# Performance work log

Measured on AMD Instinct MI355X. Metric: run time of the kernel, lower is better.

The kernel has to match this reference:

```python
import jax, jax.numpy as jnp
import numpy as np

NUM_HEADS = 8

def dwconv(x, w, b, pad):
    # depthwise conv: x [B, C, H, W], w [C, 1, k, k], groups=C
    y = jax.lax.conv_general_dilated(
        x, w, window_strides=(1, 1), padding=[(pad, pad), (pad, pad)],
        feature_group_count=x.shape[1], dimension_numbers=('NCHW', 'OIHW', 'NCHW'))
    return y + b[None, :, None, None]


def setup_inputs() -> dict:
    key = jax.random.key(0)
    ks = jax.random.split(key, 12)
    B, H, W = 32, 28, 28
    C = 512
    N = 1 + H * W
    Ch = C // NUM_HEADS  # 64
    s = lambda k, shp, fan: jax.random.normal(k, shp, jnp.float32) * (fan ** -0.5)
    return {
        'x': jax.random.normal(ks[0], (B, N, C), jnp.float32),
        'qkv_w': s(ks[1], (3 * C, C), C),
        'qkv_b': jnp.zeros((3 * C,), jnp.float32),
        'proj_w': s(ks[2], (C, C), C),
        'proj_b': jnp.zeros((C,), jnp.float32),
        'w3': s(ks[3], (2 * Ch, 1, 3, 3), 9),
        'b3': jnp.zeros((2 * Ch,), jnp.float32),
        'w5': s(ks[4], (3 * Ch, 1, 5, 5), 25),
        'b5': jnp.zeros((3 * Ch,), jnp.float32),
        'w7': s(ks[5], (3 * Ch, 1, 7, 7), 49),
        'b7': jnp.zeros((3 * Ch,), jnp.float32),
        'H': H,
        'W': W,
    }


def reference(x, qkv_w, qkv_b, proj_w, proj_b, w3, b3, w5, b5, w7, b7, H, W):
    B, N, C = x.shape
    h = NUM_HEADS
    Ch = C // h
    scale = Ch ** -0.5
    # qkv projection -> q, k, v each [B, h, N, Ch]
    qkv = (x @ qkv_w.T + qkv_b).reshape(B, N, 3, h, Ch).transpose(2, 0, 3, 1, 4)
    q, k, v = qkv[0], qkv[1], qkv[2]
    # factorized attention: softmax over tokens on k, then (k^T v) then q @ ...
    k_sm = jax.nn.softmax(k, axis=2)
    kv = jnp.einsum('bhnc,bhnd->bhcd', k_sm, v)          # [B,h,Ch,Ch]
    factor_att = jnp.einsum('bhnc,bhcd->bhnd', q, kv)    # [B,h,N,Ch]
    # conv relative position encoding (CRPE) on image tokens only
    q_img = q[:, :, 1:, :]                               # [B,h,HW,Ch]
    v_img = v[:, :, 1:, :].transpose(0, 1, 3, 2).reshape(B, h * Ch, H, W)
    splits = np.cumsum([2 * Ch, 3 * Ch, 3 * Ch])[:-1]
    v1, v2, v3 = jnp.split(v_img, splits, axis=1)
    conv_v = jnp.concatenate(
        [dwconv(v1, w3, b3, 1), dwconv(v2, w5, b5, 2), dwconv(v3, w7, b7, 3)], axis=1)
    conv_v = conv_v.reshape(B, h, Ch, H * W).transpose(0, 1, 3, 2)  # [B,h,HW,Ch]
    EV = q_img * conv_v
    crpe = jnp.pad(EV, ((0, 0), (0, 0), (1, 0), (0, 0)))  # zero row for cls token
    out = scale * factor_att + crpe
    out = out.transpose(0, 2, 1, 3).reshape(B, N, C)
    return out @ proj_w.T + proj_b
```

## Files before the change

### kernel.cpp

```cpp
#include <hip/hip_runtime.h>
#include <cstdint>
#include <cstddef>


typedef unsigned short u16;

#define HEADS 8
#define CHD   64
#define CDIM  512
#define NTOK  785
#define BATCH 32
#define MROWS (BATCH * NTOK)
#define MPAD  25344
#define QKVN  1536
#define IMGHW 784
#define KVSPLIT 7

typedef float  f32x4  __attribute__((ext_vector_type(4)));
typedef __bf16 bf16x8 __attribute__((ext_vector_type(8)));

__device__ __forceinline__ u16 f2bf(float f) {
  union { float f; uint32_t u; } x; x.f = f;
  uint32_t r = x.u + 0x7fffu + ((x.u >> 16) & 1u);
  return (u16)(r >> 16);
}
__device__ __forceinline__ float bf2f(u16 u) {
  union { uint32_t u; float f; } x; x.u = ((uint32_t)u) << 16;
  return x.f;
}
__device__ __forceinline__ float bflo(uint32_t u) { return bf2f((u16)(u & 0xffffu)); }
__device__ __forceinline__ float bfhi(uint32_t u) { return bf2f((u16)(u >> 16)); }
__device__ __forceinline__ uint32_t pk2(float a, float b) {
#if __has_builtin(__builtin_amdgcn_cvt_pk_bf16_f32)
  auto v = __builtin_amdgcn_cvt_pk_bf16_f32(a, b);
  union { decltype(v) v2; uint32_t u; } cv; cv.v2 = v; return cv.u;
#else
  return (uint32_t)f2bf(a) | ((uint32_t)f2bf(b) << 16);
#endif
}

__global__ __launch_bounds__(256)
void casts_kernel(const float* __restrict__ x, u16* __restrict__ xb,
                  const float* __restrict__ w1, u16* __restrict__ w1b,
                  const float* __restrict__ w2, u16* __restrict__ w2b) {
  const int N1 = MROWS * CDIM / 4, N2 = QKVN * CDIM / 4, N3 = CDIM * CDIM / 4;
  int i = blockIdx.x * 256 + threadIdx.x;
  const float* src; u16* dst;
  if (i < N1)           { src = x;  dst = xb;  }
  else if (i < N1 + N2) { i -= N1;  src = w1; dst = w1b; }
  else if (i < N1 + N2 + N3) { i -= N1 + N2; src = w2; dst = w2b; }
  else return;
  float4 v = reinterpret_cast<const float4*>(src)[i];
  uint2 o; o.x = pk2(v.x, v.y); o.y = pk2(v.z, v.w);
  reinterpret_cast<uint2*>(dst)[i] = o;
}

__device__ __forceinline__ void gld_lds16(const u16* g, u16* l) {
  __builtin_amdgcn_global_load_lds((__attribute__((address_space(1))) void*)g,
                                   (__attribute__((address_space(3))) void*)l,
                                   16, 0, 0);
}

template <int OUTBF16>
__global__ __launch_bounds__(512)
void gemm_bt(const u16* __restrict__ A, const u16* __restrict__ W,
             const float* __restrict__ bias, void* __restrict__ Cout,
             int Mstore, int N, int K, int nMt, int nNt) {
  __shared__ __align__(16) u16 lsA[2][256 * 32];
  __shared__ __align__(16) u16 lsB[2][128 * 32];
  const int flat = blockIdx.x;
  const int xcd = flat & 7, idx = flat >> 3;
  const int nt = idx % nNt;
  const int mt = (idx / nNt) * 8 + xcd;
  if (mt >= nMt) return;
  const int tile_m = mt * 256, tile_n = nt * 128;

  const int tid  = threadIdx.x;
  const int wave = tid >> 6, lane = tid & 63;
  const int quad = lane >> 4, l16 = lane & 15;
  const int wm = (wave & 3) * 64, wn = (wave >> 2) * 64;

  const int srow = tid >> 2;
  const int scol = ((tid & 3) ^ ((tid >> 3) & 3)) * 8;
  const int ldst = tid * 8;

  auto stage = [&](int kt, int buf) {
    const int kc = kt * 32 + scol;
#pragma unroll
    for (int s = 0; s < 2; ++s)
      gld_lds16(A + (size_t)(tile_m + s * 128 + srow) * K + kc,
                &lsA[buf][s * 4096 + ldst]);
    gld_lds16(W + (size_t)(tile_n + srow) * K + kc, &lsB[buf][ldst]);
  };

  f32x4 acc[4][4] = {};

  stage(0, 0);
  __syncthreads();

  const int KT = K >> 5;
  const int pch = (quad ^ ((l16 >> 1) & 3)) * 8;
#pragma unroll 2
  for (int t = 0; t < KT; ++t) {
    const int cur = t & 1;
    if (t + 1 < KT) stage(t + 1, cur ^ 1);
    bf16x8 af[4], bfr[4];
#pragma unroll
    for (int i = 0; i < 4; ++i) {
      af[i]  = *reinterpret_cast<const bf16x8*>(
          &lsA[cur][(wm + i * 16 + l16) * 32 + pch]);
      bfr[i] = *reinterpret_cast<const bf16x8*>(
          &lsB[cur][(wn + i * 16 + l16) * 32 + pch]);
    }
#pragma unroll
    for (int i = 0; i < 4; ++i)
#pragma unroll
      for (int j = 0; j < 4; ++j)
        acc[i][j] = __builtin_amdgcn_mfma_f32_16x16x32_bf16(
            af[i], bfr[j], acc[i][j], 0, 0, 0);
    __syncthreads();
  }

#pragma unroll
  for (int i = 0; i < 4; ++i) {
    const int mbase = tile_m + wm + i * 16 + quad * 4;
#pragma unroll
    for (int j = 0; j < 4; ++j) {
      const int n  = tile_n + wn + j * 16 + l16;
      const float bv = bias[n];
      const float v0 = acc[i][j][0] + bv, v1 = acc[i][j][1] + bv;
      const float v2 = acc[i][j][2] + bv, v3 = acc[i][j][3] + bv;
      if (OUTBF16) {
        u16* cp = reinterpret_cast<u16*>(Cout) + (size_t)mbase * N + n;
        const uint32_t p01 = pk2(v0, v1), p23 = pk2(v2, v3);
        if (mbase + 0 < Mstore) cp[0]            = (u16)p01;
        if (mbase + 1 < Mstore) cp[(size_t)N]    = (u16)(p01 >> 16);
        if (mbase + 2 < Mstore) cp[(size_t)N*2]  = (u16)p23;
        if (mbase + 3 < Mstore) cp[(size_t)N*3]  = (u16)(p23 >> 16);
      } else {
        float* cp = reinterpret_cast<float*>(Cout) + (size_t)mbase * N + n;
        if (mbase + 0 < Mstore) cp[0]           = v0;
        if (mbase + 1 < Mstore) cp[(size_t)N]   = v1;
        if (mbase + 2 < Mstore) cp[(size_t)N*2] = v2;
        if (mbase + 3 < Mstore) cp[(size_t)N*3] = v3;
      }
    }
  }
}

__device__ __forceinline__ void kv_part(
    const u16* __restrict__ qkv, float* __restrict__ kvpart,
    float* __restrict__ kvsum, int bh, int split,
    float* __restrict__ e_s, float* __restrict__ v_s) {
  const int b = bh >> 3, h = bh & 7;
  const int n_start = split * 113;
  const int n_end = min(NTOK, n_start + 113);
  const int t = threadIdx.x;
  const int d = t & 63, cq = t >> 6;
  const int c4 = (t & 15) * 4;
  const u16* kbase = qkv + (size_t)(b * NTOK) * QKVN + CDIM + h * CHD;
  const u16* vbase = kbase + CDIM;
  float acc[16];
#pragma unroll
  for (int i = 0; i < 16; ++i) acc[i] = 0.f;
  f32x4 sp4 = {0.f, 0.f, 0.f, 0.f};

  for (int n0 = n_start; n0 < n_end; n0 += 32) {
    const int nc = min(32, n_end - n0);
    __syncthreads();
    for (int i4 = t; i4 < nc * 16; i4 += 256) {
      const int nl = i4 >> 4;
      const uint2 kk = *reinterpret_cast<const uint2*>(
          &kbase[(size_t)(n0 + nl) * QKVN + c4]);
      const uint2 vv = *reinterpret_cast<const uint2*>(
          &vbase[(size_t)(n0 + nl) * QKVN + c4]);
      f32x4 e4, v4;
      e4[0] = __expf(bflo(kk.x)); e4[1] = __expf(bfhi(kk.x));
      e4[2] = __expf(bflo(kk.y)); e4[3] = __expf(bfhi(kk.y));
      v4[0] = bflo(vv.x); v4[1] = bfhi(vv.x);
      v4[2] = bflo(vv.y); v4[3] = bfhi(vv.y);
      *reinterpret_cast<f32x4*>(&e_s[nl * 64 + c4]) = e4;
      *reinterpret_cast<f32x4*>(&v_s[nl * 64 + c4]) = v4;
      sp4 += e4;
    }
    __syncthreads();
    for (int nl = 0; nl < nc; ++nl) {
      const float vv = v_s[nl * 64 + d];
      const f32x4* ep = reinterpret_cast<const f32x4*>(&e_s[nl * 64 + cq * 16]);
      const f32x4 e0 = ep[0], e1 = ep[1], e2 = ep[2], e3 = ep[3];
      acc[0] += e0[0] * vv; acc[1] += e0[1] * vv; acc[2] += e0[2] * vv; acc[3] += e0[3] * vv;
      acc[4] += e1[0] * vv; acc[5] += e1[1] * vv; acc[6] += e1[2] * vv; acc[7] += e1[3] * vv;
      acc[8] += e2[0] * vv; acc[9] += e2[1] * vv; acc[10] += e2[2] * vv; acc[11] += e2[3] * vv;
      acc[12] += e3[0] * vv; acc[13] += e3[1] * vv; acc[14] += e3[2] * vv; acc[15] += e3[3] * vv;
    }
  }
#pragma unroll
  for (int i = 0; i < 16; ++i) {
    const int c = cq * 16 + i;
    kvpart[(((size_t)bh * KVSPLIT + split) * 64 + c) * 64 + d] = acc[i];
  }
  __syncthreads();
  *reinterpret_cast<f32x4*>(&e_s[t * 4]) = sp4;
  __syncthreads();
  if (t < 64) {
    float S = 0.f;
#pragma unroll
    for (int m = 0; m < 16; ++m)
      S += e_s[((t >> 2) + 16 * m) * 4 + (t & 3)];
    kvsum[((size_t)bh * KVSPLIT + split) * 64 + t] = S;
  }
}

__global__ __launch_bounds__(256)
void kv_reduce_kernel(const float* __restrict__ kvpart, const float* __restrict__ kvsum,
                      u16* __restrict__ kvT) {
  const int bh = blockIdx.x;
  const int t = threadIdx.x;
  const int d = t & 63, cq = t >> 6;
#pragma unroll
  for (int cc = 0; cc < 16; ++cc) {
    const int c = cq * 16 + cc;
    float s = 0.f, S = 0.f;
#pragma unroll
    for (int sp = 0; sp < KVSPLIT; ++sp) {
      s += kvpart[(((size_t)bh * KVSPLIT + sp) * 64 + c) * 64 + d];
      S += kvsum[((size_t)bh * KVSPLIT + sp) * 64 + c];
    }
    kvT[(size_t)bh * 4096 + d * 64 + c] = f2bf(s / S);
  }
}

template <int KS>
__device__ __forceinline__ void conv_head(
    const u16* __restrict__ qkv, const float* __restrict__ wgt,
    const float* __restrict__ bias, int b, int head, int hh, int yt,
    u16* __restrict__ evbuf, u16* __restrict__ ls, float* __restrict__ wls) {
  constexpr int PAD = KS / 2;
  constexpr int RIN = 4 + 2 * PAD;
  const int t = threadIdx.x;
  const int y0 = yt * 4;
  const u16* vimg = qkv + (size_t)(b * NTOK + 1) * QKVN + 2 * CDIM + head * 64;
  for (int i = t; i < 64 * KS * KS; i += 256)
    wls[i] = wgt[hh * 64 * KS * KS + i];
  const int c8 = (t & 7) * 8;
  for (int pi = t >> 3; pi < RIN * 28; pi += 32) {
    const int ry = pi / 28, rx = pi - ry * 28;
    const int yy = y0 - PAD + ry;
    uint4 val = {0, 0, 0, 0};
    if (yy >= 0 && yy < 28)
      val = *reinterpret_cast<const uint4*>(vimg + (size_t)(yy * 28 + rx) * QKVN + c8);
    *reinterpret_cast<uint4*>(ls + pi * 64 + c8) = val;
  }
  __syncthreads();
  const int d = t & 63, yl = t >> 6;
  float wr[KS * KS];
#pragma unroll
  for (int i = 0; i < KS * KS; ++i) wr[i] = wls[d * KS * KS + i];
  const float bv = bias[hh * 64 + d];
  float acc[28];
#pragma unroll
  for (int x = 0; x < 28; ++x) acc[x] = bv;
#pragma unroll
  for (int xx = 0; xx < 28; ++xx) {
    float col[KS];
#pragma unroll
    for (int r = 0; r < KS; ++r)
      col[r] = bf2f(ls[((yl + r) * 28 + xx) * 64 + d]);
#pragma unroll
    for (int j = 0; j < KS; ++j) {
      const int x = xx + PAD - j;
      if (x >= 0 && x < 28) {
#pragma unroll
        for (int r = 0; r < KS; ++r)
          acc[x] += col[r] * wr[r * KS + j];
      }
    }
  }
  const int p0 = (y0 + yl) * 28;
  const u16* qrow = qkv + (size_t)(b * NTOK + 1 + p0) * QKVN + head * 64 + d;
  u16* obase = evbuf + (((size_t)(b * 8 + head)) * IMGHW + p0) * 64 + d;
#pragma unroll
  for (int x = 0; x < 28; ++x) {
    const float ev = acc[x] * bf2f(qrow[(size_t)x * QKVN]);
    obase[(size_t)x * 64] = f2bf(ev);
  }
}

__global__ __launch_bounds__(256)
void kv_conv_kernel(const u16* __restrict__ qkv, float* __restrict__ kvpart,
                    float* __restrict__ kvsum,
                    const float* __restrict__ w3, const float* __restrict__ b3,
                    const float* __restrict__ w5, const float* __restrict__ b5,
                    const float* __restrict__ w7, const float* __restrict__ b7,
                    u16* __restrict__ evbuf) {
  __shared__ __align__(16) char smem[10 * 28 * 64 * 2 + 64 * 49 * 4];
  const int y = blockIdx.y;
  if (y < KVSPLIT) {
    float* e_s = reinterpret_cast<float*>(smem);
    float* v_s = e_s + 32 * 64;
    kv_part(qkv, kvpart, kvsum, blockIdx.x, y, e_s, v_s);
  } else {
    u16* ls = reinterpret_cast<u16*>(smem);
    float* wls = reinterpret_cast<float*>(smem + 10 * 28 * 64 * 2);
    const int b = blockIdx.x >> 3, h = blockIdx.x & 7, yt = y - KVSPLIT;
    if (h < 2)      conv_head<3>(qkv, w3, b3, b, h, h,     yt, evbuf, ls, wls);
    else if (h < 5) conv_head<5>(qkv, w5, b5, b, h, h - 2, yt, evbuf, ls, wls);
    else            conv_head<7>(qkv, w7, b7, b, h, h - 5, yt, evbuf, ls, wls);
  }
}

__global__ __launch_bounds__(256)
void combine_kernel(const u16* __restrict__ qkv, const u16* __restrict__ kvT,
                    const u16* __restrict__ evbuf, u16* __restrict__ attn) {
  __shared__ __align__(16) float sa[128 * 64];
  const int bh = blockIdx.x;
  const int b = bh >> 3, h = bh & 7;
  const int t = threadIdx.x;
  const int wave = t >> 6, lane = t & 63;
  const int quad = lane >> 4, l16 = lane & 15;
  const int tokbase = blockIdx.y * 256 + wave * 64;

  const u16* kvb = kvT + (size_t)bh * 4096;
  bf16x8 bfr[4][2];
#pragma unroll
  for (int j = 0; j < 4; ++j)
#pragma unroll
    for (int kk = 0; kk < 2; ++kk)
      bfr[j][kk] = *reinterpret_cast<const bf16x8*>(
          &kvb[(j * 16 + l16) * 64 + kk * 32 + quad * 8]);

  bf16x8 af[4][2];
#pragma unroll
  for (int i = 0; i < 4; ++i) {
    const int tok = min(tokbase + i * 16 + l16, NTOK - 1);
    const u16* qrow = qkv + (size_t)(b * NTOK + tok) * QKVN + h * CHD;
    af[i][0] = *reinterpret_cast<const bf16x8*>(&qrow[quad * 8]);
    af[i][1] = *reinterpret_cast<const bf16x8*>(&qrow[32 + quad * 8]);
  }

  f32x4 acc[4][4] = {};
#pragma unroll
  for (int kk = 0; kk < 2; ++kk)
#pragma unroll
    for (int i = 0; i < 4; ++i)
#pragma unroll
      for (int j = 0; j < 4; ++j)
        acc[i][j] = __builtin_amdgcn_mfma_f32_16x16x32_bf16(af[i][kk], bfr[j][kk], acc[i][j], 0, 0, 0);

  const float scale = 0.125f;
  const u16* evb = evbuf + (size_t)bh * IMGHW * 64;
#pragma unroll
  for (int half = 0; half < 2; ++half) {
    if ((wave >> 1) == half) {
      const int rbase = (wave & 1) * 64;
#pragma unroll
      for (int i = 0; i < 4; ++i)
#pragma unroll
        for (int rr = 0; rr < 4; ++rr) {
          const int rl = rbase + i * 16 + quad * 4 + rr;
#pragma unroll
          for (int j = 0; j < 4; ++j) {
            const int dd = j * 16 + l16;
            sa[rl * 64 + (((dd >> 2) ^ (rl & 15)) * 4) + (dd & 3)] =
                scale * acc[i][j][rr];
          }
        }
    }
    __syncthreads();
    {
      const int rl = t >> 1;
      const int tok = blockIdx.y * 256 + half * 128 + rl;
      if (tok < NTOK) {
        u16* orow = attn + (size_t)(b * NTOK + tok) * CDIM + h * CHD;
        const int cb = (t & 1) * 8;
#pragma unroll
        for (int c2 = 0; c2 < 4; ++c2) {
          const int ch0 = cb + c2 * 2;
          const f32x4 v0 = *reinterpret_cast<const f32x4*>(
              &sa[rl * 64 + ((ch0 ^ (rl & 15)) * 4)]);
          const f32x4 v1 = *reinterpret_cast<const f32x4*>(
              &sa[rl * 64 + (((ch0 + 1) ^ (rl & 15)) * 4)]);
          float o0 = v0[0], o1 = v0[1], o2 = v0[2], o3 = v0[3];
          float o4 = v1[0], o5 = v1[1], o6 = v1[2], o7 = v1[3];
          if (tok > 0) {
            const uint4 ev = *reinterpret_cast<const uint4*>(
                &evb[(size_t)(tok - 1) * 64 + ch0 * 4]);
            o0 += bflo(ev.x); o1 += bfhi(ev.x);
            o2 += bflo(ev.y); o3 += bfhi(ev.y);
            o4 += bflo(ev.z); o5 += bfhi(ev.z);
            o6 += bflo(ev.w); o7 += bfhi(ev.w);
          }
          uint4 ow;
          ow.x = pk2(o0, o1); ow.y = pk2(o2, o3);
          ow.z = pk2(o4, o5); ow.w = pk2(o6, o7);
          *reinterpret_cast<uint4*>(&orow[ch0 * 4]) = ow;
        }
      }
    }
    __syncthreads();
  }
}

extern "C" void kernel_launch(void* const* d_in, const int* in_sizes, int n_in,
                              void* d_out, int out_size, void* d_ws, size_t ws_size,
                              hipStream_t stream) {
  const float* x      = (const float*)d_in[0];
  const float* qkv_w  = (const float*)d_in[1];
  const float* qkv_b  = (const float*)d_in[2];
  const float* proj_w = (const float*)d_in[3];
  const float* proj_b = (const float*)d_in[4];
  const float* w3 = (const float*)d_in[5];
  const float* b3 = (const float*)d_in[6];
  const float* w5 = (const float*)d_in[7];
  const float* b5 = (const float*)d_in[8];
  const float* w7 = (const float*)d_in[9];
  const float* b7 = (const float*)d_in[10];
  float* out = (float*)d_out;

  char* p = (char*)d_ws;
  u16* xb    = (u16*)p;   p += (size_t)MPAD * CDIM * 2;
  u16* wqb   = (u16*)p;   p += (size_t)QKVN * CDIM * 2;
  u16* wpb   = (u16*)p;   p += (size_t)CDIM * CDIM * 2;
  u16* qkvb  = (u16*)p;   p += (size_t)MPAD * QKVN * 2;
  float* kvsum = (float*)p; p += (size_t)256 * KVSPLIT * 64 * 4;
  u16* kvT   = (u16*)p;   p += (size_t)256 * 64 * 64 * 2;
  float* kvpart = (float*)p; p += (size_t)256 * KVSPLIT * 64 * 64 * 4;
  u16* attn  = (u16*)p;   p += (size_t)MPAD * CDIM * 2;
  u16* evbuf = xb;

  {
    const int total = MROWS * CDIM / 4 + QKVN * CDIM / 4 + CDIM * CDIM / 4;
    casts_kernel<<<(total + 255) / 256, 256, 0, stream>>>(x, xb, qkv_w, wqb, proj_w, wpb);
  }
  gemm_bt<1><<<13 * 8 * 12, 512, 0, stream>>>(xb, wqb, qkv_b, qkvb,
                                              MPAD, QKVN, CDIM, 99, 12);
  kv_conv_kernel<<<dim3(256, KVSPLIT + 7), 256, 0, stream>>>(
      qkvb, kvpart, kvsum, w3, b3, w5, b5, w7, b7, evbuf);
  kv_reduce_kernel<<<256, 256, 0, stream>>>(kvpart, kvsum, kvT);
  combine_kernel<<<dim3(256, 4), 256, 0, stream>>>(qkvb, kvT, evbuf, attn);
  gemm_bt<0><<<13 * 8 * 4, 512, 0, stream>>>(attn, wpb, proj_b, out,
                                             MROWS, CDIM, CDIM, 99, 4);
}
```

Baseline: 313.1 us.

## Accumulate KV partials with atomics and use a 4x4 register tile

Instead of writing seven per-split KV partial matrices and summing them in the reduce kernel, each split block atomically adds its partial into a single zeroed accumulator, and the zeroing is folded into the cast kernel. The inner product loop switches from a 16x1 tile per thread to a 4x4 outer-product tile built from vector LDS loads, which cuts LDS traffic per FMA. This removes about 7MB of partial-buffer writes and reads, at the cost of float atomics, which contend across splits and make the summation order nondeterministic.

```diff
diff --git a/kernel.cpp b/kernel.cpp
--- a/kernel.cpp
+++ b/kernel.cpp
@@ -42,13 +42,21 @@
 __global__ __launch_bounds__(256)
 void casts_kernel(const float* __restrict__ x, u16* __restrict__ xb,
                   const float* __restrict__ w1, u16* __restrict__ w1b,
-                  const float* __restrict__ w2, u16* __restrict__ w2b) {
+                  const float* __restrict__ w2, u16* __restrict__ w2b,
+                  float* __restrict__ zbuf) {
   const int N1 = MROWS * CDIM / 4, N2 = QKVN * CDIM / 4, N3 = CDIM * CDIM / 4;
+  const int N4 = (256 * 64 * 64 + 256 * 64) / 4;
   int i = blockIdx.x * 256 + threadIdx.x;
   const float* src; u16* dst;
   if (i < N1)           { src = x;  dst = xb;  }
   else if (i < N1 + N2) { i -= N1;  src = w1; dst = w1b; }
   else if (i < N1 + N2 + N3) { i -= N1 + N2; src = w2; dst = w2b; }
+  else if (i < N1 + N2 + N3 + N4) {
+    i -= N1 + N2 + N3;
+    float4 z = {0.f, 0.f, 0.f, 0.f};
+    reinterpret_cast<float4*>(zbuf)[i] = z;
+    return;
+  }
   else return;
   float4 v = reinterpret_cast<const float4*>(src)[i];
   uint2 o; o.x = pk2(v.x, v.y); o.y = pk2(v.z, v.w);
@@ -149,20 +157,18 @@
 }
 
 __device__ __forceinline__ void kv_part(
-    const u16* __restrict__ qkv, float* __restrict__ kvpart,
+    const u16* __restrict__ qkv, float* __restrict__ kvacc,
     float* __restrict__ kvsum, int bh, int split,
     float* __restrict__ e_s, float* __restrict__ v_s) {
   const int b = bh >> 3, h = bh & 7;
   const int n_start = split * 113;
   const int n_end = min(NTOK, n_start + 113);
   const int t = threadIdx.x;
-  const int d = t & 63, cq = t >> 6;
   const int c4 = (t & 15) * 4;
+  const int d4 = (t >> 4) * 4;
   const u16* kbase = qkv + (size_t)(b * NTOK) * QKVN + CDIM + h * CHD;
   const u16* vbase = kbase + CDIM;
-  float acc[16];
-#pragma unroll
-  for (int i = 0; i < 16; ++i) acc[i] = 0.f;
+  f32x4 acc[4] = {};
   f32x4 sp4 = {0.f, 0.f, 0.f, 0.f};
 
   for (int n0 = n_start; n0 < n_end; n0 += 32) {
@@ -185,20 +191,20 @@
     }
     __syncthreads();
     for (int nl = 0; nl < nc; ++nl) {
-      const float vv = v_s[nl * 64 + d];
-      const f32x4* ep = reinterpret_cast<const f32x4*>(&e_s[nl * 64 + cq * 16]);
-      const f32x4 e0 = ep[0], e1 = ep[1], e2 = ep[2], e3 = ep[3];
-      acc[0] += e0[0] * vv; acc[1] += e0[1] * vv; acc[2] += e0[2] * vv; acc[3] += e0[3] * vv;
-      acc[4] += e1[0] * vv; acc[5] += e1[1] * vv; acc[6] += e1[2] * vv; acc[7] += e1[3] * vv;
-      acc[8] += e2[0] * vv; acc[9] += e2[1] * vv; acc[10] += e2[2] * vv; acc[11] += e2[3] * vv;
-      acc[12] += e3[0] * vv; acc[13] += e3[1] * vv; acc[14] += e3[2] * vv; acc[15] += e3[3] * vv;
-    }
-  }
-#pragma unroll
-  for (int i = 0; i < 16; ++i) {
-    const int c = cq * 16 + i;
-    kvpart[(((size_t)bh * KVSPLIT + split) * 64 + c) * 64 + d] = acc[i];
-  }
+      const f32x4 e4 = *reinterpret_cast<const f32x4*>(&e_s[nl * 64 + c4]);
+      const f32x4 v4 = *reinterpret_cast<const f32x4*>(&v_s[nl * 64 + d4]);
+      acc[0] += e4[0] * v4;
+      acc[1] += e4[1] * v4;
+      acc[2] += e4[2] * v4;
+      acc[3] += e4[3] * v4;
+    }
+  }
+  float* kb = kvacc + ((size_t)bh * 64 + c4) * 64 + d4;
+#pragma unroll
+  for (int ci = 0; ci < 4; ++ci)
+#pragma unroll
+    for (int di = 0; di < 4; ++di)
+      atomicAdd(&kb[ci * 64 + di], acc[ci][di]);
   __syncthreads();
   *reinterpret_cast<f32x4*>(&e_s[t * 4]) = sp4;
   __syncthreads();
@@ -207,12 +213,12 @@
 #pragma unroll
     for (int m = 0; m < 16; ++m)
       S += e_s[((t >> 2) + 16 * m) * 4 + (t & 3)];
-    kvsum[((size_t)bh * KVSPLIT + split) * 64 + t] = S;
+    atomicAdd(&kvsum[(size_t)bh * 64 + t], S);
   }
 }
 
 __global__ __launch_bounds__(256)
-void kv_reduce_kernel(const float* __restrict__ kvpart, const float* __restrict__ kvsum,
+void kv_reduce_kernel(const float* __restrict__ kvacc, const float* __restrict__ kvsum,
                       u16* __restrict__ kvT) {
   const int bh = blockIdx.x;
   const int t = threadIdx.x;
@@ -220,12 +226,8 @@
 #pragma unroll
   for (int cc = 0; cc < 16; ++cc) {
     const int c = cq * 16 + cc;
-    float s = 0.f, S = 0.f;
-#pragma unroll
-    for (int sp = 0; sp < KVSPLIT; ++sp) {
-      s += kvpart[(((size_t)bh * KVSPLIT + sp) * 64 + c) * 64 + d];
-      S += kvsum[((size_t)bh * KVSPLIT + sp) * 64 + c];
-    }
+    const float s = kvacc[((size_t)bh * 64 + c) * 64 + d];
+    const float S = kvsum[(size_t)bh * 64 + c];
     kvT[(size_t)bh * 4096 + d * 64 + c] = f2bf(s / S);
   }
 }
@@ -287,7 +289,7 @@
 }
 
 __global__ __launch_bounds__(256)
-void kv_conv_kernel(const u16* __restrict__ qkv, float* __restrict__ kvpart,
+void kv_conv_kernel(const u16* __restrict__ qkv, float* __restrict__ kvacc,
                     float* __restrict__ kvsum,
                     const float* __restrict__ w3, const float* __restrict__ b3,
                     const float* __restrict__ w5, const float* __restrict__ b5,
@@ -298,7 +300,7 @@
   if (y < KVSPLIT) {
     float* e_s = reinterpret_cast<float*>(smem);
     float* v_s = e_s + 32 * 64;
-    kv_part(qkv, kvpart, kvsum, blockIdx.x, y, e_s, v_s);
+    kv_part(qkv, kvacc, kvsum, blockIdx.x, y, e_s, v_s);
   } else {
     u16* ls = reinterpret_cast<u16*>(smem);
     float* wls = reinterpret_cast<float*>(smem + 10 * 28 * 64 * 2);
@@ -422,21 +424,23 @@
   u16* wqb   = (u16*)p;   p += (size_t)QKVN * CDIM * 2;
   u16* wpb   = (u16*)p;   p += (size_t)CDIM * CDIM * 2;
   u16* qkvb  = (u16*)p;   p += (size_t)MPAD * QKVN * 2;
-  float* kvsum = (float*)p; p += (size_t)256 * KVSPLIT * 64 * 4;
+  float* kvacc = (float*)p; p += (size_t)256 * 64 * 64 * 4;
+  float* kvsum = (float*)p; p += (size_t)256 * 64 * 4;
   u16* kvT   = (u16*)p;   p += (size_t)256 * 64 * 64 * 2;
-  float* kvpart = (float*)p; p += (size_t)256 * KVSPLIT * 64 * 64 * 4;
   u16* attn  = (u16*)p;   p += (size_t)MPAD * CDIM * 2;
   u16* evbuf = xb;
 
   {
-    const int total = MROWS * CDIM / 4 + QKVN * CDIM / 4 + CDIM * CDIM / 4;
-    casts_kernel<<<(total + 255) / 256, 256, 0, stream>>>(x, xb, qkv_w, wqb, proj_w, wpb);
+    const int total = MROWS * CDIM / 4 + QKVN * CDIM / 4 + CDIM * CDIM / 4 +
+                      (256 * 64 * 64 + 256 * 64) / 4;
+    casts_kernel<<<(total + 255) / 256, 256, 0, stream>>>(
+        x, xb, qkv_w, wqb, proj_w, wpb, kvacc);
   }
   gemm_bt<1><<<13 * 8 * 12, 512, 0, stream>>>(xb, wqb, qkv_b, qkvb,
                                               MPAD, QKVN, CDIM, 99, 12);
   kv_conv_kernel<<<dim3(256, KVSPLIT + 7), 256, 0, stream>>>(
-      qkvb, kvpart, kvsum, w3, b3, w5, b5, w7, b7, evbuf);
-  kv_reduce_kernel<<<256, 256, 0, stream>>>(kvpart, kvsum, kvT);
+      qkvb, kvacc, kvsum, w3, b3, w5, b5, w7, b7, evbuf);
+  kv_reduce_kernel<<<256, 256, 0, stream>>>(kvacc, kvsum, kvT);
   combine_kernel<<<dim3(256, 4), 256, 0, stream>>>(qkvb, kvT, evbuf, attn);
   gemm_bt<0><<<13 * 8 * 4, 512, 0, stream>>>(attn, wpb, proj_b, out,
                                              MROWS, CDIM, CDIM, 99, 4);
```

Result: slower. 366.8 us (+17.1%).
